# Kernel optimization log

Hardware: AMD Instinct MI355X
Metric: run time of the kernel (lower is better)

The kernel has to match this reference:

```python
import jax, jax.numpy as jnp
import numpy as np

L, B, F, D = 12, 2048, 6144, 768

def setup_inputs() -> dict:
    key = jax.random.key(0)
    k1, k2, k3 = jax.random.split(key, 3)
    acts = jax.random.normal(k1, (L, B, F), dtype=jnp.float32)
    # decoder weights for target layer: stacked per source layer, [L, F, D]
    W = jax.random.normal(k2, (L, F, D), dtype=jnp.float32) * 0.02
    bias = jax.random.normal(k3, (L, D), dtype=jnp.float32) * 0.01
    return {"acts": acts, "W": W, "bias": bias, "layer_idx": 11}

def reference(acts, W, bias, layer_idx):
    # decode(): sum over src_layer <= layer_idx of Linear(a[src], W[src->tgt], b[src->tgt])
    n = layer_idx + 1  # static Python int -> static slice
    a = acts[:n]       # [n, B, F]
    w = W[:n]          # [n, F, D]
    b = bias[:n]       # [n, D]
    # fused accumulation of all per-source-layer GEMMs
    recon = jnp.einsum('lbf,lfd->bd', a, w) + jnp.sum(b, axis=0)  # [B, D]
    return recon
```

## Files before the change

kernel.cpp:

```cpp
#include <hip/hip_runtime.h>
#include <hip/hip_bf16.h>

#define NB 2048
#define NF 6144
#define ND 768
#define NT (NF / 64)

typedef __attribute__((ext_vector_type(8))) __bf16 bf16x8;
typedef __attribute__((ext_vector_type(4))) float f32x4;

__device__ __forceinline__ char* lds_addr(char* base, int row, int k) {
  const int blk = ((k >> 3) ^ (row & 7) ^ ((row >> 2) & 7)) & 7;
  return base + row * 128 + (blk << 4) + ((k & 7) << 1);
}

#define BAR()                                              \
  do {                                                     \
    asm volatile("s_waitcnt lgkmcnt(0)" ::: "memory");     \
    __builtin_amdgcn_sched_barrier(0);                     \
    __builtin_amdgcn_s_barrier();                          \
    __builtin_amdgcn_sched_barrier(0);                     \
  } while (0)

__global__ __launch_bounds__(256) void bias_init_kernel(
    const float* __restrict__ bias, const int* __restrict__ lidx,
    float* __restrict__ out) {
  int n = lidx[0] + 1;
  int i = blockIdx.x * 256 + threadIdx.x;
  if (i >= NB * ND) return;
  int d = i % ND;
  float s = 0.f;
  for (int l = 0; l < n; ++l) s += bias[l * ND + d];
  out[i] = s;
}

__global__ __launch_bounds__(256, 2) void gemm_kernel(
    const float* __restrict__ acts, const float* __restrict__ W,
    const int* __restrict__ lidx, float* __restrict__ out) {
  const int l = blockIdx.z;
  if (l > lidx[0]) return;

  const int brow = blockIdx.x * 128;
  const int ncol = blockIdx.y * 128;

  __shared__ char cbuf[2][32768];

  const int tid = threadIdx.x;
  const int lane = tid & 63;
  const int wid = tid >> 6;
  const int wrow = (wid >> 1) * 64;
  const int wcol = (wid & 1) * 64;

  f32x4 acc[4][4];
#pragma unroll
  for (int i = 0; i < 4; ++i)
#pragma unroll
    for (int j = 0; j < 4; ++j) acc[i][j] = (f32x4){0.f, 0.f, 0.f, 0.f};

  const int s_arow = tid >> 3;
  const int s_ak = (tid & 7) * 8;
  const int s_bd = (tid & 31) * 4;
  const int s_bk = (tid >> 5) * 8;

  const float* Aptr =
      acts + (size_t)l * NB * NF + (size_t)(brow + s_arow) * NF + s_ak;
  const float* Bptr =
      W + (size_t)l * NF * ND + (size_t)s_bk * ND + (ncol + s_bd);

  float4 av[4][2];
  float4 bv[8];

  auto LOADS = [&](int kb) {
#pragma unroll
    for (int p = 0; p < 4; ++p) {
      av[p][0] = *(const float4*)(Aptr + (size_t)(32 * p) * NF + kb);
      av[p][1] = *(const float4*)(Aptr + (size_t)(32 * p) * NF + kb + 4);
    }
#pragma unroll
    for (int j = 0; j < 8; ++j)
      bv[j] = *(const float4*)(Bptr + (size_t)(kb + j) * ND);
  };

  auto STORE = [&](int buf) {
    char* cA_ = cbuf[buf];
    char* cB_ = cbuf[buf] + 16384;
#pragma unroll
    for (int p = 0; p < 4; ++p) {
      bf16x8 h;
      h[0] = (__bf16)av[p][0].x; h[1] = (__bf16)av[p][0].y;
      h[2] = (__bf16)av[p][0].z; h[3] = (__bf16)av[p][0].w;
      h[4] = (__bf16)av[p][1].x; h[5] = (__bf16)av[p][1].y;
      h[6] = (__bf16)av[p][1].z; h[7] = (__bf16)av[p][1].w;
      *(bf16x8*)lds_addr(cA_, s_arow + 32 * p, s_ak) = h;
    }
#pragma unroll
    for (int dd = 0; dd < 4; ++dd) {
      bf16x8 h;
#pragma unroll
      for (int j = 0; j < 8; ++j) h[j] = (__bf16)bv[j][dd];
      *(bf16x8*)lds_addr(cB_, s_bd + dd, s_bk) = h;
    }
  };

  auto KSTEP = [&](int buf, int s) {
    char* cA_ = cbuf[buf];
    char* cB_ = cbuf[buf] + 16384;
    const int kk = s * 32 + (lane >> 4) * 8;
    bf16x8 aF[4], bF[4];
#pragma unroll
    for (int mi = 0; mi < 4; ++mi)
      aF[mi] = *(const bf16x8*)lds_addr(cA_, wrow + mi * 16 + (lane & 15), kk);
#pragma unroll
    for (int ni = 0; ni < 4; ++ni)
      bF[ni] = *(const bf16x8*)lds_addr(cB_, wcol + ni * 16 + (lane & 15), kk);
#pragma unroll
    for (int mi = 0; mi < 4; ++mi)
#pragma unroll
      for (int ni = 0; ni < 4; ++ni)
        acc[mi][ni] = __builtin_amdgcn_mfma_f32_16x16x32_bf16(
            aF[mi], bF[ni], acc[mi][ni], 0, 0, 0);
  };

  LOADS(0);
  STORE(0);
  LOADS(64);

  for (int t = 0; t < NT; ++t) {
    BAR();
    const int cur = t & 1;
    KSTEP(cur, 0);
    KSTEP(cur, 1);
    if (t + 1 < NT) STORE(cur ^ 1);
    if (t + 2 < NT) LOADS((t + 2) * 64);
  }

  const int orow = brow + wrow + ((lane >> 4) << 2);
  const int ocol = ncol + wcol + (lane & 15);
#pragma unroll
  for (int mi = 0; mi < 4; ++mi)
#pragma unroll
    for (int ni = 0; ni < 4; ++ni)
#pragma unroll
      for (int j = 0; j < 4; ++j)
        atomicAdd(out + (size_t)(orow + mi * 16 + j) * ND + (ocol + ni * 16),
                  acc[mi][ni][j]);
}

extern "C" void kernel_launch(void* const* d_in, const int* in_sizes, int n_in,
                              void* d_out, int out_size, void* d_ws, size_t ws_size,
                              hipStream_t stream) {
  const float* acts = (const float*)d_in[0];
  const float* W    = (const float*)d_in[1];
  const float* bias = (const float*)d_in[2];
  const int*   lidx = (const int*)d_in[3];
  float* out = (float*)d_out;

  const int L = in_sizes[0] / (NB * NF);

  bias_init_kernel<<<dim3((NB * ND + 255) / 256), 256, 0, stream>>>(bias, lidx, out);
  gemm_kernel<<<dim3(NB / 128, ND / 128, L), 256, 0, stream>>>(acts, W, lidx, out);
}
```

Measured before the change: 511.4 us.

## Halve K tile to 32, raise occupancy to 3 blocks, swizzle workgroups across XCDs

Shrinks the K-step from 64 to 32, which halves LDS usage per block and the register staging buffers, and raises launch bounds to 3 blocks per CU so more memory latency can be hidden. Also flattens the grid to 1D and remaps block IDs so that consecutive workgroups on the same XCD share tiles, aiming for better L2 reuse. In exchange there are twice as many barriers per K, and each sync covers less MFMA work. The B stores to LDS become narrower 8-byte writes.

```diff
diff --git a/kernel.cpp b/kernel.cpp
--- a/kernel.cpp
+++ b/kernel.cpp
@@ -4,14 +4,16 @@
 #define NB 2048
 #define NF 6144
 #define ND 768
-#define NT (NF / 64)
+#define BK 32
+#define NT (NF / BK)
 
+typedef __attribute__((ext_vector_type(4))) __bf16 bf16x4;
 typedef __attribute__((ext_vector_type(8))) __bf16 bf16x8;
 typedef __attribute__((ext_vector_type(4))) float f32x4;
 
 __device__ __forceinline__ char* lds_addr(char* base, int row, int k) {
-  const int blk = ((k >> 3) ^ (row & 7) ^ ((row >> 2) & 7)) & 7;
-  return base + row * 128 + (blk << 4) + ((k & 7) << 1);
+  const int blk = ((k >> 3) ^ (row & 3) ^ ((row >> 2) & 3)) & 3;
+  return base + row * 64 + (blk << 4) + ((k & 7) << 1);
 }
 
 #define BAR()                                              \
@@ -34,16 +36,21 @@
   out[i] = s;
 }
 
-__global__ __launch_bounds__(256, 2) void gemm_kernel(
+__global__ __launch_bounds__(256, 3) void gemm_kernel(
     const float* __restrict__ acts, const float* __restrict__ W,
-    const int* __restrict__ lidx, float* __restrict__ out) {
-  const int l = blockIdx.z;
+    const int* __restrict__ lidx, float* __restrict__ out, int nwg) {
+  const int chunk = nwg >> 3;
+  const int swz = (blockIdx.x & 7) * chunk + (blockIdx.x >> 3);
+  const int bx = swz & 15;
+  const int rem = swz >> 4;
+  const int by = rem % 6;
+  const int l = rem / 6;
   if (l > lidx[0]) return;
 
-  const int brow = blockIdx.x * 128;
-  const int ncol = blockIdx.y * 128;
+  const int brow = bx * 128;
+  const int ncol = by * 128;
 
-  __shared__ char cbuf[2][32768];
+  __shared__ char cbuf[2][16384];
 
   const int tid = threadIdx.x;
   const int lane = tid & 63;
@@ -57,55 +64,55 @@
 #pragma unroll
     for (int j = 0; j < 4; ++j) acc[i][j] = (f32x4){0.f, 0.f, 0.f, 0.f};
 
-  const int s_arow = tid >> 3;
-  const int s_ak = (tid & 7) * 8;
+  const int s_arow = tid >> 2;
+  const int s_ak = (tid & 3) * 8;
   const int s_bd = (tid & 31) * 4;
-  const int s_bk = (tid >> 5) * 8;
+  const int s_bk = (tid >> 5) * 4;
 
   const float* Aptr =
       acts + (size_t)l * NB * NF + (size_t)(brow + s_arow) * NF + s_ak;
   const float* Bptr =
       W + (size_t)l * NF * ND + (size_t)s_bk * ND + (ncol + s_bd);
 
-  float4 av[4][2];
-  float4 bv[8];
+  float4 av[2][2];
+  float4 bv[4];
 
   auto LOADS = [&](int kb) {
 #pragma unroll
-    for (int p = 0; p < 4; ++p) {
-      av[p][0] = *(const float4*)(Aptr + (size_t)(32 * p) * NF + kb);
-      av[p][1] = *(const float4*)(Aptr + (size_t)(32 * p) * NF + kb + 4);
+    for (int p = 0; p < 2; ++p) {
+      av[p][0] = *(const float4*)(Aptr + (size_t)(64 * p) * NF + kb);
+      av[p][1] = *(const float4*)(Aptr + (size_t)(64 * p) * NF + kb + 4);
     }
 #pragma unroll
-    for (int j = 0; j < 8; ++j)
+    for (int j = 0; j < 4; ++j)
       bv[j] = *(const float4*)(Bptr + (size_t)(kb + j) * ND);
   };
 
   auto STORE = [&](int buf) {
     char* cA_ = cbuf[buf];
-    char* cB_ = cbuf[buf] + 16384;
+    char* cB_ = cbuf[buf] + 8192;
 #pragma unroll
-    for (int p = 0; p < 4; ++p) {
+    for (int p = 0; p < 2; ++p) {
       bf16x8 h;
       h[0] = (__bf16)av[p][0].x; h[1] = (__bf16)av[p][0].y;
       h[2] = (__bf16)av[p][0].z; h[3] = (__bf16)av[p][0].w;
       h[4] = (__bf16)av[p][1].x; h[5] = (__bf16)av[p][1].y;
       h[6] = (__bf16)av[p][1].z; h[7] = (__bf16)av[p][1].w;
-      *(bf16x8*)lds_addr(cA_, s_arow + 32 * p, s_ak) = h;
+      *(bf16x8*)lds_addr(cA_, s_arow + 64 * p, s_ak) = h;
     }
 #pragma unroll
     for (int dd = 0; dd < 4; ++dd) {
-      bf16x8 h;
-#pragma unroll
-      for (int j = 0; j < 8; ++j) h[j] = (__bf16)bv[j][dd];
-      *(bf16x8*)lds_addr(cB_, s_bd + dd, s_bk) = h;
+      bf16x4 h;
+      h[0] = (__bf16)bv[0][dd]; h[1] = (__bf16)bv[1][dd];
+      h[2] = (__bf16)bv[2][dd]; h[3] = (__bf16)bv[3][dd];
+      *(bf16x4*)lds_addr(cB_, s_bd + dd, s_bk) = h;
     }
   };
 
-  auto KSTEP = [&](int buf, int s) {
+  auto KSTEP = [&](int buf) {
     char* cA_ = cbuf[buf];
-    char* cB_ = cbuf[buf] + 16384;
-    const int kk = s * 32 + (lane >> 4) * 8;
+    char* cB_ = cbuf[buf] + 8192;
+    const int kk = (lane >> 4) * 8;
     bf16x8 aF[4], bF[4];
 #pragma unroll
     for (int mi = 0; mi < 4; ++mi)
@@ -123,15 +130,14 @@
 
   LOADS(0);
   STORE(0);
-  LOADS(64);
+  LOADS(BK);
 
   for (int t = 0; t < NT; ++t) {
     BAR();
     const int cur = t & 1;
-    KSTEP(cur, 0);
-    KSTEP(cur, 1);
+    KSTEP(cur);
     if (t + 1 < NT) STORE(cur ^ 1);
-    if (t + 2 < NT) LOADS((t + 2) * 64);
+    if (t + 2 < NT) LOADS((t + 2) * BK);
   }
 
   const int orow = brow + wrow + ((lane >> 4) << 2);
@@ -156,7 +162,8 @@
   float* out = (float*)d_out;
 
   const int L = in_sizes[0] / (NB * NF);
+  const int nwg = (NB / 128) * (ND / 128) * L;
 
   bias_init_kernel<<<dim3((NB * ND + 255) / 256), 256, 0, stream>>>(bias, lidx, out);
-  gemm_kernel<<<dim3(NB / 128, ND / 128, L), 256, 0, stream>>>(acts, W, lidx, out);
+  gemm_kernel<<<dim3(nwg), 256, 0, stream>>>(acts, W, lidx, out, nwg);
 }
```

Result: slower. 612.1 us (+19.7%).

## Enlarge GEMM tiles to 256x192 with split-K and XCD-aware block swizzle

Applied to the files above, without the earlier changes.

Moves the per-layer GEMM from 128x128 tiles with 256 threads to 256x192 tiles with 512 threads. Each wave now computes a 64x96 sub-tile, and the K dimension is split in two halves that both accumulate through the existing atomics. A 1D grid with a remap that groups blocks by blockIdx&7 decides which blocks share an XCD. The aim is to cut how often the fp32 activations and weights are re-read from global memory, and to improve L2 locality. The cost is more dynamic LDS per block, which likely allows only one block per CU, plus more registers per wave and twice as many output atomics from the split-K.

```diff
diff --git a/kernel.cpp b/kernel.cpp
--- a/kernel.cpp
+++ b/kernel.cpp
@@ -4,7 +4,16 @@
 #define NB 2048
 #define NF 6144
 #define ND 768
-#define NT (NF / 64)
+#define BM 256
+#define BN 192
+#define BK 64
+#define SPLITK 2
+#define KHALF (NF / SPLITK)
+#define NT (KHALF / BK)
+
+#define ABYTES (BM * 128)
+#define BBYTES (BN * 128)
+#define BUFBYTES (ABYTES + BBYTES)
 
 typedef __attribute__((ext_vector_type(8))) __bf16 bf16x8;
 typedef __attribute__((ext_vector_type(4))) float f32x4;
@@ -34,38 +43,46 @@
   out[i] = s;
 }
 
-__global__ __launch_bounds__(256, 2) void gemm_kernel(
+__global__ __launch_bounds__(512, 2) void gemm_kernel(
     const float* __restrict__ acts, const float* __restrict__ W,
-    const int* __restrict__ lidx, float* __restrict__ out) {
-  const int l = blockIdx.z;
+    const int* __restrict__ lidx, float* __restrict__ out, int nwg) {
+  extern __shared__ char cbuf[];
+
+  const int chunk = nwg >> 3;
+  const int swz = (blockIdx.x & 7) * chunk + (blockIdx.x >> 3);
+  const int m = swz & 7;
+  int rem = swz >> 3;
+  const int ks = rem & 1; rem >>= 1;
+  const int by = rem & 3; rem >>= 2;
+  const int l = rem;
   if (l > lidx[0]) return;
 
-  const int brow = blockIdx.x * 128;
-  const int ncol = blockIdx.y * 128;
-
-  __shared__ char cbuf[2][32768];
+  const int brow = m * BM;
+  const int ncol = by * BN;
+  const int k0 = ks * KHALF;
 
   const int tid = threadIdx.x;
   const int lane = tid & 63;
   const int wid = tid >> 6;
   const int wrow = (wid >> 1) * 64;
-  const int wcol = (wid & 1) * 64;
+  const int wcol = (wid & 1) * 96;
 
-  f32x4 acc[4][4];
+  f32x4 acc[4][6];
 #pragma unroll
   for (int i = 0; i < 4; ++i)
 #pragma unroll
-    for (int j = 0; j < 4; ++j) acc[i][j] = (f32x4){0.f, 0.f, 0.f, 0.f};
+    for (int j = 0; j < 6; ++j) acc[i][j] = (f32x4){0.f, 0.f, 0.f, 0.f};
 
   const int s_arow = tid >> 3;
   const int s_ak = (tid & 7) * 8;
-  const int s_bd = (tid & 31) * 4;
-  const int s_bk = (tid >> 5) * 8;
+  const bool bstage = tid < 384;
+  const int s_bd = (tid % 48) * 4;
+  const int s_bk = (tid / 48) * 8;
 
   const float* Aptr =
-      acts + (size_t)l * NB * NF + (size_t)(brow + s_arow) * NF + s_ak;
+      acts + (size_t)l * NB * NF + (size_t)(brow + s_arow) * NF + k0 + s_ak;
   const float* Bptr =
-      W + (size_t)l * NF * ND + (size_t)s_bk * ND + (ncol + s_bd);
+      W + (size_t)l * NF * ND + (size_t)(k0 + s_bk) * ND + (ncol + s_bd);
 
   float4 av[4][2];
   float4 bv[8];
@@ -73,17 +90,19 @@
   auto LOADS = [&](int kb) {
 #pragma unroll
     for (int p = 0; p < 4; ++p) {
-      av[p][0] = *(const float4*)(Aptr + (size_t)(32 * p) * NF + kb);
-      av[p][1] = *(const float4*)(Aptr + (size_t)(32 * p) * NF + kb + 4);
+      av[p][0] = *(const float4*)(Aptr + (size_t)(64 * p) * NF + kb);
+      av[p][1] = *(const float4*)(Aptr + (size_t)(64 * p) * NF + kb + 4);
     }
+    if (bstage) {
 #pragma unroll
-    for (int j = 0; j < 8; ++j)
-      bv[j] = *(const float4*)(Bptr + (size_t)(kb + j) * ND);
+      for (int j = 0; j < 8; ++j)
+        bv[j] = *(const float4*)(Bptr + (size_t)(kb + j) * ND);
+    }
   };
 
   auto STORE = [&](int buf) {
-    char* cA_ = cbuf[buf];
-    char* cB_ = cbuf[buf] + 16384;
+    char* cA_ = cbuf + (size_t)buf * BUFBYTES;
+    char* cB_ = cA_ + ABYTES;
 #pragma unroll
     for (int p = 0; p < 4; ++p) {
       bf16x8 h;
@@ -91,39 +110,41 @@
       h[2] = (__bf16)av[p][0].z; h[3] = (__bf16)av[p][0].w;
       h[4] = (__bf16)av[p][1].x; h[5] = (__bf16)av[p][1].y;
       h[6] = (__bf16)av[p][1].z; h[7] = (__bf16)av[p][1].w;
-      *(bf16x8*)lds_addr(cA_, s_arow + 32 * p, s_ak) = h;
+      *(bf16x8*)lds_addr(cA_, s_arow + 64 * p, s_ak) = h;
     }
+    if (bstage) {
 #pragma unroll
-    for (int dd = 0; dd < 4; ++dd) {
-      bf16x8 h;
+      for (int dd = 0; dd < 4; ++dd) {
+        bf16x8 h;
 #pragma unroll
-      for (int j = 0; j < 8; ++j) h[j] = (__bf16)bv[j][dd];
-      *(bf16x8*)lds_addr(cB_, s_bd + dd, s_bk) = h;
+        for (int j = 0; j < 8; ++j) h[j] = (__bf16)bv[j][dd];
+        *(bf16x8*)lds_addr(cB_, s_bd + dd, s_bk) = h;
+      }
     }
   };
 
   auto KSTEP = [&](int buf, int s) {
-    char* cA_ = cbuf[buf];
-    char* cB_ = cbuf[buf] + 16384;
+    char* cA_ = cbuf + (size_t)buf * BUFBYTES;
+    char* cB_ = cA_ + ABYTES;
     const int kk = s * 32 + (lane >> 4) * 8;
-    bf16x8 aF[4], bF[4];
+    bf16x8 aF[4], bF[6];
 #pragma unroll
     for (int mi = 0; mi < 4; ++mi)
       aF[mi] = *(const bf16x8*)lds_addr(cA_, wrow + mi * 16 + (lane & 15), kk);
 #pragma unroll
-    for (int ni = 0; ni < 4; ++ni)
+    for (int ni = 0; ni < 6; ++ni)
       bF[ni] = *(const bf16x8*)lds_addr(cB_, wcol + ni * 16 + (lane & 15), kk);
 #pragma unroll
     for (int mi = 0; mi < 4; ++mi)
 #pragma unroll
-      for (int ni = 0; ni < 4; ++ni)
+      for (int ni = 0; ni < 6; ++ni)
         acc[mi][ni] = __builtin_amdgcn_mfma_f32_16x16x32_bf16(
             aF[mi], bF[ni], acc[mi][ni], 0, 0, 0);
   };
 
   LOADS(0);
   STORE(0);
-  LOADS(64);
+  LOADS(BK);
 
   for (int t = 0; t < NT; ++t) {
     BAR();
@@ -131,7 +152,7 @@
     KSTEP(cur, 0);
     KSTEP(cur, 1);
     if (t + 1 < NT) STORE(cur ^ 1);
-    if (t + 2 < NT) LOADS((t + 2) * 64);
+    if (t + 2 < NT) LOADS((t + 2) * BK);
   }
 
   const int orow = brow + wrow + ((lane >> 4) << 2);
@@ -139,7 +160,7 @@
 #pragma unroll
   for (int mi = 0; mi < 4; ++mi)
 #pragma unroll
-    for (int ni = 0; ni < 4; ++ni)
+    for (int ni = 0; ni < 6; ++ni)
 #pragma unroll
       for (int j = 0; j < 4; ++j)
         atomicAdd(out + (size_t)(orow + mi * 16 + j) * ND + (ocol + ni * 16),
@@ -156,7 +177,12 @@
   float* out = (float*)d_out;
 
   const int L = in_sizes[0] / (NB * NF);
+  const int nwg = (NB / BM) * SPLITK * (ND / BN) * L;
+
+  hipFuncSetAttribute((const void*)gemm_kernel,
+                      hipFuncAttributeMaxDynamicSharedMemorySize,
+                      2 * BUFBYTES);
 
   bias_init_kernel<<<dim3((NB * ND + 255) / 256), 256, 0, stream>>>(bias, lidx, out);
-  gemm_kernel<<<dim3(NB / 128, ND / 128, L), 256, 0, stream>>>(acts, W, lidx, out);
+  gemm_kernel<<<dim3(nwg), 512, 2 * BUFBYTES, stream>>>(acts, W, lidx, out, nwg);
 }
```

New measurement: 575.9 us. 12.6% more time.

## Single-buffer LDS for 3 blocks/CU, XCD-aware block swizzle, defer B loads

Applied to the files above, without the earlier changes.

Replaces the double-buffered LDS tile with a single buffer and adds a second barrier per k-step, so LDS use drops to 32KB and three blocks can run per CU (launch bounds raised to 3). B-tile global loads move into the store phase, which shortens register live ranges. The 3D grid becomes 1D with a chunked swizzle that maps consecutive blocks on each XCD to neighbouring tiles, meant to improve L2 reuse. In exchange, the extra barrier serialises the loads and MFMA work inside each block and hides less latency there, relying on the other resident blocks to cover it.

```diff
diff --git a/kernel.cpp b/kernel.cpp
--- a/kernel.cpp
+++ b/kernel.cpp
@@ -4,7 +4,8 @@
 #define NB 2048
 #define NF 6144
 #define ND 768
-#define NT (NF / 64)
+#define BK 64
+#define NT (NF / BK)
 
 typedef __attribute__((ext_vector_type(8))) __bf16 bf16x8;
 typedef __attribute__((ext_vector_type(4))) float f32x4;
@@ -34,16 +35,22 @@
   out[i] = s;
 }
 
-__global__ __launch_bounds__(256, 2) void gemm_kernel(
+__global__ __launch_bounds__(256, 3) void gemm_kernel(
     const float* __restrict__ acts, const float* __restrict__ W,
-    const int* __restrict__ lidx, float* __restrict__ out) {
-  const int l = blockIdx.z;
+    const int* __restrict__ lidx, float* __restrict__ out, int nwg) {
+  const int chunk = nwg >> 3;
+  const int swz = (blockIdx.x & 7) * chunk + (blockIdx.x >> 3);
+  const int m = swz & 15;
+  const int rem = swz >> 4;
+  const int by = rem % 6;
+  const int l = rem / 6;
   if (l > lidx[0]) return;
 
-  const int brow = blockIdx.x * 128;
-  const int ncol = blockIdx.y * 128;
+  const int brow = m * 128;
+  const int ncol = by * 128;
 
-  __shared__ char cbuf[2][32768];
+  __shared__ char cA[16384];
+  __shared__ char cB[16384];
 
   const int tid = threadIdx.x;
   const int lane = tid & 63;
@@ -68,22 +75,20 @@
       W + (size_t)l * NF * ND + (size_t)s_bk * ND + (ncol + s_bd);
 
   float4 av[4][2];
-  float4 bv[8];
 
-  auto LOADS = [&](int kb) {
+  auto ALOADS = [&](int kb) {
 #pragma unroll
     for (int p = 0; p < 4; ++p) {
       av[p][0] = *(const float4*)(Aptr + (size_t)(32 * p) * NF + kb);
       av[p][1] = *(const float4*)(Aptr + (size_t)(32 * p) * NF + kb + 4);
     }
+  };
+
+  auto STORE = [&](int kb) {
+    float4 bv[8];
 #pragma unroll
     for (int j = 0; j < 8; ++j)
       bv[j] = *(const float4*)(Bptr + (size_t)(kb + j) * ND);
-  };
-
-  auto STORE = [&](int buf) {
-    char* cA_ = cbuf[buf];
-    char* cB_ = cbuf[buf] + 16384;
 #pragma unroll
     for (int p = 0; p < 4; ++p) {
       bf16x8 h;
@@ -91,28 +96,26 @@
       h[2] = (__bf16)av[p][0].z; h[3] = (__bf16)av[p][0].w;
       h[4] = (__bf16)av[p][1].x; h[5] = (__bf16)av[p][1].y;
       h[6] = (__bf16)av[p][1].z; h[7] = (__bf16)av[p][1].w;
-      *(bf16x8*)lds_addr(cA_, s_arow + 32 * p, s_ak) = h;
+      *(bf16x8*)lds_addr(cA, s_arow + 32 * p, s_ak) = h;
     }
 #pragma unroll
     for (int dd = 0; dd < 4; ++dd) {
       bf16x8 h;
 #pragma unroll
       for (int j = 0; j < 8; ++j) h[j] = (__bf16)bv[j][dd];
-      *(bf16x8*)lds_addr(cB_, s_bd + dd, s_bk) = h;
+      *(bf16x8*)lds_addr(cB, s_bd + dd, s_bk) = h;
     }
   };
 
-  auto KSTEP = [&](int buf, int s) {
-    char* cA_ = cbuf[buf];
-    char* cB_ = cbuf[buf] + 16384;
+  auto KSTEP = [&](int s) {
     const int kk = s * 32 + (lane >> 4) * 8;
     bf16x8 aF[4], bF[4];
 #pragma unroll
     for (int mi = 0; mi < 4; ++mi)
-      aF[mi] = *(const bf16x8*)lds_addr(cA_, wrow + mi * 16 + (lane & 15), kk);
+      aF[mi] = *(const bf16x8*)lds_addr(cA, wrow + mi * 16 + (lane & 15), kk);
 #pragma unroll
     for (int ni = 0; ni < 4; ++ni)
-      bF[ni] = *(const bf16x8*)lds_addr(cB_, wcol + ni * 16 + (lane & 15), kk);
+      bF[ni] = *(const bf16x8*)lds_addr(cB, wcol + ni * 16 + (lane & 15), kk);
 #pragma unroll
     for (int mi = 0; mi < 4; ++mi)
 #pragma unroll
@@ -121,17 +124,17 @@
             aF[mi], bF[ni], acc[mi][ni], 0, 0, 0);
   };
 
-  LOADS(0);
+  ALOADS(0);
   STORE(0);
-  LOADS(64);
+  ALOADS(BK);
 
   for (int t = 0; t < NT; ++t) {
     BAR();
-    const int cur = t & 1;
-    KSTEP(cur, 0);
-    KSTEP(cur, 1);
-    if (t + 1 < NT) STORE(cur ^ 1);
-    if (t + 2 < NT) LOADS((t + 2) * 64);
+    KSTEP(0);
+    KSTEP(1);
+    BAR();
+    if (t + 1 < NT) STORE((t + 1) * BK);
+    if (t + 2 < NT) ALOADS((t + 2) * BK);
   }
 
   const int orow = brow + wrow + ((lane >> 4) << 2);
@@ -156,7 +159,8 @@
   float* out = (float*)d_out;
 
   const int L = in_sizes[0] / (NB * NF);
+  const int nwg = (NB / 128) * (ND / 128) * L;
 
   bias_init_kernel<<<dim3((NB * ND + 255) / 256), 256, 0, stream>>>(bias, lidx, out);
-  gemm_kernel<<<dim3(NB / 128, ND / 128, L), 256, 0, stream>>>(acts, W, lidx, out);
+  gemm_kernel<<<dim3(nwg), 256, 0, stream>>>(acts, W, lidx, out, nwg);
 }
```

Result: slower. 538.9 us (+5.4%).
